# Kernel tuning notes

Measured on AMD Instinct MI355X. Metric: run time of the kernel, lower is better.

## Reference

```python
import jax, jax.numpy as jnp
import numpy as np

HIDDEN = 2048
N_HEADS = 16
N_KV_HEADS = 4
HEAD_DIM = 128
EPS = 1e-6


def rms_norm(x, w, eps=EPS):
    xf = x.astype(jnp.float32)
    var = jnp.mean(xf * xf, axis=-1, keepdims=True)
    return w * (xf * jax.lax.rsqrt(var + eps)).astype(x.dtype)


def setup_inputs() -> dict:
    key = jax.random.key(0)
    ks = jax.random.split(key, 8)
    B, S, S_ENC = 4, 2048, 1024
    inner = N_HEADS * HEAD_DIM
    kv_dim = N_KV_HEADS * HEAD_DIM
    s = 0.02
    return {
        "hidden_states": jax.random.normal(ks[0], (B, S, HIDDEN), jnp.float32),
        "encoder_hidden_states": jax.random.normal(ks[1], (B, S_ENC, HIDDEN), jnp.float32),
        "Wq": jax.random.normal(ks[2], (HIDDEN, inner), jnp.float32) * s,
        "Wk": jax.random.normal(ks[3], (HIDDEN, kv_dim), jnp.float32) * s,
        "Wv": jax.random.normal(ks[4], (HIDDEN, kv_dim), jnp.float32) * s,
        "Wo": jax.random.normal(ks[5], (inner, HIDDEN), jnp.float32) * s,
        "q_norm_w": jnp.ones((HEAD_DIM,), jnp.float32),
        "k_norm_w": jnp.ones((HEAD_DIM,), jnp.float32),
    }


def reference(hidden_states, encoder_hidden_states, Wq, Wk, Wv, Wo, q_norm_w, k_norm_w):
    B, S, _ = hidden_states.shape
    S_enc = encoder_hidden_states.shape[1]
    groups = N_HEADS // N_KV_HEADS
    scale = 1.0 / (HEAD_DIM ** 0.5)

    q = (hidden_states @ Wq).reshape(B, S, N_HEADS, HEAD_DIM)
    k = (encoder_hidden_states @ Wk).reshape(B, S_enc, N_KV_HEADS, HEAD_DIM)
    v = (encoder_hidden_states @ Wv).reshape(B, S_enc, N_KV_HEADS, HEAD_DIM)

    q = rms_norm(q, q_norm_w)
    k = rms_norm(k, k_norm_w)

    # GQA expand kv heads to full heads
    k = jnp.repeat(k, groups, axis=2)  # [B, S_enc, H, D]
    v = jnp.repeat(v, groups, axis=2)

    # non-causal SDPA
    scores = jnp.einsum("bqhd,bkhd->bhqk", q, k) * scale
    probs = jax.nn.softmax(scores, axis=-1)
    out = jnp.einsum("bhqk,bkhd->bqhd", probs, v)

    out = out.reshape(B, S, N_HEADS * HEAD_DIM)
    return out @ Wo
```

## Files before the change

### kernel.cpp

```cpp
#include <hip/hip_runtime.h>
#include <hip/hip_bf16.h>


typedef short  bf16x8 __attribute__((ext_vector_type(8)));
typedef float  f32x4  __attribute__((ext_vector_type(4)));
typedef unsigned short us;

__device__ __forceinline__ us f2bf(float f) {
    union { float f; unsigned u; } v; v.f = f;
    unsigned r = v.u + 0x7fffu + ((v.u >> 16) & 1u);
    return (us)(r >> 16);
}
__device__ __forceinline__ float bf2f(us u) {
    union { unsigned u; float f; } v; v.u = ((unsigned)u) << 16;
    return v.f;
}

typedef __attribute__((address_space(3))) unsigned int lds_u32;
typedef __attribute__((address_space(1))) const unsigned int glb_u32;

__device__ __forceinline__ void gl_lds16(const us* g, us* l) {
    __builtin_amdgcn_global_load_lds((glb_u32*)g, (lds_u32*)l, 16, 0, 0);
}

__launch_bounds__(256)
__global__ void cvt_kernel(const float* __restrict__ in, us* __restrict__ out) {
    size_t i = ((size_t)blockIdx.x * 256 + threadIdx.x) * 8;
    float4 v0 = *(const float4*)(in + i);
    float4 v1 = *(const float4*)(in + i + 4);
    bf16x8 h;
    h[0] = f2bf(v0.x); h[1] = f2bf(v0.y); h[2] = f2bf(v0.z); h[3] = f2bf(v0.w);
    h[4] = f2bf(v1.x); h[5] = f2bf(v1.y); h[6] = f2bf(v1.z); h[7] = f2bf(v1.w);
    *(bf16x8*)(out + i) = h;
}

__launch_bounds__(256)
__global__ void tpose_kernel(const float* __restrict__ in, us* __restrict__ out,
                             int K, int N) {
    __shared__ us tile[64][65];
    const int n0 = blockIdx.x * 64;
    const int k0 = blockIdx.y * 64;
    const int t  = threadIdx.x;
    const int r  = t >> 4;
    const int c4 = (t & 15) * 4;
    #pragma unroll
    for (int rr = 0; rr < 64; rr += 16) {
        float4 v = *(const float4*)(in + (size_t)(k0 + r + rr) * N + n0 + c4);
        tile[r + rr][c4 + 0] = f2bf(v.x);
        tile[r + rr][c4 + 1] = f2bf(v.y);
        tile[r + rr][c4 + 2] = f2bf(v.z);
        tile[r + rr][c4 + 3] = f2bf(v.w);
    }
    __syncthreads();
    #pragma unroll
    for (int rr = 0; rr < 64; rr += 16) {
        ushort4 o;
        o.x = tile[c4 + 0][r + rr];
        o.y = tile[c4 + 1][r + rr];
        o.z = tile[c4 + 2][r + rr];
        o.w = tile[c4 + 3][r + rr];
        *(ushort4*)(out + (size_t)(n0 + r + rr) * K + k0 + c4) = o;
    }
}

template <int EPI>
__launch_bounds__(256)
__global__ void gemm2_kernel(const us* __restrict__ A,
                             const us* __restrict__ Bt,
                             void* __restrict__ Out,
                             void* __restrict__ Out2,
                             int M, int N, int K) {
    __shared__ __align__(16) us As[128 * 64];
    __shared__ __align__(16) us Bs[128 * 64];

    const int tid  = threadIdx.x;
    const int lane = tid & 63;
    const int wv   = tid >> 6;

    const int nwg  = gridDim.x * gridDim.y;
    const int bid  = blockIdx.y * gridDim.x + blockIdx.x;
    const int cpx  = nwg >> 3;
    const int swz  = (bid & 7) * cpx + (bid >> 3);
    const int row0 = (swz / gridDim.x) * 128;
    const int n0   = (swz % gridDim.x) * 128;

    const int wr   = (wv >> 1) * 64;
    const int wc   = (wv & 1) * 64;
    const int la   = lane & 15;
    const int lg   = lane >> 4;

    const int srow = lane >> 3;
    const int scol = (((lane & 7) ^ srow) * 8);

    const int bs0 = ((0 + lg) ^ (la & 7)) * 8;
    const int bs1 = ((4 + lg) ^ (la & 7)) * 8;

    f32x4 acc[4][4] = {};

    for (int k0 = 0; k0 < K; k0 += 64) {
        #pragma unroll
        for (int r = 0; r < 4; ++r) {
            int brow = wv * 32 + r * 8;
            gl_lds16(Bt + (size_t)(n0 + brow + srow) * K + k0 + scol, &Bs[brow * 64]);
        }
        #pragma unroll
        for (int r = 0; r < 4; ++r) {
            int arow = wv * 32 + r * 8;
            gl_lds16(A + (size_t)(row0 + arow + srow) * K + k0 + scol, &As[arow * 64]);
        }
        __syncthreads();

        bf16x8 af[2][4], bg[2][4];
        #pragma unroll
        for (int i = 0; i < 4; ++i) {
            af[0][i] = *(const bf16x8*)&As[(wr + i * 16 + la) * 64 + bs0];
            af[1][i] = *(const bf16x8*)&As[(wr + i * 16 + la) * 64 + bs1];
        }
        #pragma unroll
        for (int j = 0; j < 4; ++j) {
            bg[0][j] = *(const bf16x8*)&Bs[(wc + j * 16 + la) * 64 + bs0];
            bg[1][j] = *(const bf16x8*)&Bs[(wc + j * 16 + la) * 64 + bs1];
        }
        #pragma unroll
        for (int kk = 0; kk < 2; ++kk)
            #pragma unroll
            for (int i = 0; i < 4; ++i)
                #pragma unroll
                for (int j = 0; j < 4; ++j)
                    acc[i][j] = __builtin_amdgcn_mfma_f32_16x16x32_bf16(af[kk][i], bg[kk][j], acc[i][j], 0, 0, 0);
        __syncthreads();
    }

    const int lgq = lane >> 4;
    #pragma unroll
    for (int i = 0; i < 4; ++i) {
        #pragma unroll
        for (int j = 0; j < 4; ++j) {
            #pragma unroll
            for (int r = 0; r < 4; ++r) {
                int row_g = row0 + wr + i * 16 + lgq * 4 + r;
                int col_g = n0 + wc + j * 16 + la;
                float val = acc[i][j][r];
                if (EPI == 0) {
                    ((us*)Out)[(size_t)row_g * N + col_g] = f2bf(val);
                } else if (EPI == 2) {
                    ((float*)Out)[(size_t)row_g * N + col_g] = val;
                } else {
                    if (col_g < 512) {
                        ((us*)Out)[(size_t)row_g * 512 + col_g] = f2bf(val);
                    } else {
                        int cc  = col_g - 512;
                        int b_  = row_g >> 10, s_ = row_g & 1023;
                        int kvh = cc >> 7,     d_ = cc & 127;
                        ((us*)Out2)[(((size_t)(b_ * 4 + kvh) * 128 + d_) << 10) + s_] = f2bf(val);
                    }
                }
            }
        }
    }
}

__launch_bounds__(256)
__global__ void rmsnorm_kernel(us* __restrict__ x, const float* __restrict__ w,
                               int nseg, float postscale) {
    int seg  = blockIdx.x * 4 + (threadIdx.x >> 6);
    if (seg >= nseg) return;
    int lane = threadIdx.x & 63;
    size_t base = (size_t)seg * 128 + lane * 2;
    unsigned v = *(const unsigned*)&x[base];
    float x0 = bf2f((us)(v & 0xffff));
    float x1 = bf2f((us)(v >> 16));
    float s = x0 * x0 + x1 * x1;
    #pragma unroll
    for (int m = 1; m < 64; m <<= 1) s += __shfl_xor(s, m, 64);
    float rinv = rsqrtf(s * (1.0f / 128.0f) + 1e-6f) * postscale;
    x0 = x0 * rinv * w[lane * 2];
    x1 = x1 * rinv * w[lane * 2 + 1];
    unsigned o = (unsigned)f2bf(x0) | ((unsigned)f2bf(x1) << 16);
    *(unsigned*)&x[base] = o;
}

__launch_bounds__(256, 2)
__global__ void attn_kernel(const us* __restrict__ Q,
                            const us* __restrict__ Kb,
                            const us* __restrict__ Vt,
                            us* __restrict__ Ob) {
    __shared__ __align__(16) us Klds[64 * 132];
    __shared__ __align__(16) us Vtlds[128 * 68];
    __shared__ __align__(16) us Plds[4][32 * 68];

    const int tid  = threadIdx.x;
    const int bid  = blockIdx.x;
    const int qt   = bid & 15;
    const int bh   = bid >> 4;
    const int b    = bh >> 4;
    const int h    = bh & 15;
    const int kvh  = h >> 2;

    const int lane = tid & 63;
    const int wv   = tid >> 6;
    const int la   = lane & 15;
    const int lg   = lane >> 4;
    const int lb   = lg * 8;

    const int qr0 = qt * 128 + wv * 32;

    bf16x8 aq[2][4];
    #pragma unroll
    for (int i = 0; i < 2; ++i)
        #pragma unroll
        for (int t = 0; t < 4; ++t)
            aq[i][t] = *(const bf16x8*)&Q[(size_t)(b * 2048 + qr0 + i * 16 + la) * 2048
                                          + h * 128 + t * 32 + lb];

    f32x4 oacc[2][8] = {};
    float l_part[2][4] = {};

    const us* Kbase  = Kb + (size_t)(b * 1024) * 512 + kvh * 128;
    const us* Vtbase = Vt + (size_t)(b * 4 + kvh) * 128 * 1024;

    for (int kt = 0; kt < 16; ++kt) {
        #pragma unroll
        for (int r = 0; r < 4; ++r) {
            int idx  = tid + r * 256;
            int srow = idx >> 4;
            int c8   = (idx & 15) << 3;
            uint4 v = *(const uint4*)(Kbase + (size_t)(kt * 64 + srow) * 512 + c8);
            *(uint4*)&Klds[srow * 132 + c8] = v;
        }
        #pragma unroll
        for (int r = 0; r < 4; ++r) {
            int idx  = tid + r * 256;
            int drow = idx >> 3;
            int c8   = (idx & 7) << 3;
            uint4 v = *(const uint4*)(Vtbase + (size_t)drow * 1024 + kt * 64 + c8);
            *(uint4*)&Vtlds[drow * 68 + c8] = v;
        }
        __syncthreads();

        f32x4 sacc[2][4] = {};
        __builtin_amdgcn_s_setprio(1);
        #pragma unroll
        for (int j = 0; j < 4; ++j) {
            bf16x8 bk[4];
            #pragma unroll
            for (int t = 0; t < 4; ++t)
                bk[t] = *(const bf16x8*)&Klds[(j * 16 + la) * 132 + t * 32 + lb];
            #pragma unroll
            for (int t = 0; t < 4; ++t)
                #pragma unroll
                for (int i = 0; i < 2; ++i)
                    sacc[i][j] = __builtin_amdgcn_mfma_f32_16x16x32_bf16(aq[i][t], bk[t], sacc[i][j], 0, 0, 0);
        }
        __builtin_amdgcn_s_setprio(0);

        #pragma unroll
        for (int i = 0; i < 2; ++i) {
            #pragma unroll
            for (int r = 0; r < 4; ++r) {
                float ls = 0.0f;
                #pragma unroll
                for (int j = 0; j < 4; ++j) {
                    float p = __expf(sacc[i][j][r]);
                    sacc[i][j][r] = p;
                    ls += p;
                }
                l_part[i][r] += ls;
            }
        }

        #pragma unroll
        for (int i = 0; i < 2; ++i)
            #pragma unroll
            for (int j = 0; j < 4; ++j)
                #pragma unroll
                for (int r = 0; r < 4; ++r)
                    Plds[wv][(i * 16 + lg * 4 + r) * 68 + j * 16 + la] = f2bf(sacc[i][j][r]);

        __builtin_amdgcn_s_setprio(1);
        #pragma unroll
        for (int ks = 0; ks < 2; ++ks) {
            bf16x8 pa[2];
            #pragma unroll
            for (int i = 0; i < 2; ++i)
                pa[i] = *(const bf16x8*)&Plds[wv][(i * 16 + la) * 68 + ks * 32 + lb];
            #pragma unroll
            for (int df = 0; df < 8; ++df) {
                bf16x8 bv = *(const bf16x8*)&Vtlds[(df * 16 + la) * 68 + ks * 32 + lb];
                #pragma unroll
                for (int i = 0; i < 2; ++i)
                    oacc[i][df] = __builtin_amdgcn_mfma_f32_16x16x32_bf16(pa[i], bv, oacc[i][df], 0, 0, 0);
            }
        }
        __builtin_amdgcn_s_setprio(0);
        __syncthreads();
    }

    #pragma unroll
    for (int i = 0; i < 2; ++i) {
        #pragma unroll
        for (int r = 0; r < 4; ++r) {
            float l = l_part[i][r];
            l += __shfl_xor(l, 1, 64);
            l += __shfl_xor(l, 2, 64);
            l += __shfl_xor(l, 4, 64);
            l += __shfl_xor(l, 8, 64);
            float inv = 1.0f / l;
            int row_g = b * 2048 + qr0 + i * 16 + lg * 4 + r;
            #pragma unroll
            for (int df = 0; df < 8; ++df) {
                int col_g = h * 128 + df * 16 + la;
                Ob[(size_t)row_g * 2048 + col_g] = f2bf(oacc[i][df][r] * inv);
            }
        }
    }
}

extern "C" void kernel_launch(void* const* d_in, const int* in_sizes, int n_in,
                              void* d_out, int out_size, void* d_ws, size_t ws_size,
                              hipStream_t stream) {
    const float* hidden = (const float*)d_in[0];
    const float* enc    = (const float*)d_in[1];
    const float* Wq     = (const float*)d_in[2];
    const float* Wk     = (const float*)d_in[3];
    const float* Wv     = (const float*)d_in[4];
    const float* Wo     = (const float*)d_in[5];
    const float* qw     = (const float*)d_in[6];
    const float* kw     = (const float*)d_in[7];
    float* out = (float*)d_out;

    us* ws16 = (us*)d_ws;
    us* hidden_bf = ws16;
    us* WqT       = ws16 + 16777216;
    us* Qu        = ws16 + 20971520;
    us* enc_bf    = ws16;
    us* WkT       = ws16 + 8388608;
    us* WvT       = ws16 + 9437184;
    us* WoT       = ws16 + 10485760;
    us* Kn        = ws16 + 14680064;
    us* Vt        = ws16 + 16777216;

    dim3 blk(256);
    const float scale = 0.08838834764831845f;

    cvt_kernel<<<dim3(8192), blk, 0, stream>>>(hidden, hidden_bf);
    tpose_kernel<<<dim3(32, 32), blk, 0, stream>>>(Wq, WqT, 2048, 2048);
    gemm2_kernel<0><<<dim3(16, 64), blk, 0, stream>>>(hidden_bf, WqT, Qu, nullptr, 8192, 2048, 2048);

    cvt_kernel<<<dim3(4096), blk, 0, stream>>>(enc, enc_bf);
    tpose_kernel<<<dim3(8, 32),  blk, 0, stream>>>(Wk, WkT, 2048, 512);
    tpose_kernel<<<dim3(8, 32),  blk, 0, stream>>>(Wv, WvT, 2048, 512);
    tpose_kernel<<<dim3(32, 32), blk, 0, stream>>>(Wo, WoT, 2048, 2048);
    gemm2_kernel<3><<<dim3(8, 32), blk, 0, stream>>>(enc_bf, WkT, Kn, Vt, 4096, 1024, 2048);

    rmsnorm_kernel<<<dim3(32768), blk, 0, stream>>>(Qu, qw, 8192 * 16, scale);
    rmsnorm_kernel<<<dim3(4096),  blk, 0, stream>>>(Kn, kw, 4096 * 4, 1.0f);

    attn_kernel<<<dim3(1024), blk, 0, stream>>>(Qu, Kn, Vt, Qu);

    gemm2_kernel<2><<<dim3(16, 64), blk, 0, stream>>>(Qu, WoT, out, nullptr, 8192, 2048, 2048);
}
```

Measured before the change: 374.4 us.

## Read V directly from global memory, fold log2e into Q scale, pack bf16 converts

Stops staging the transposed V tile in shared memory; each lane now loads its V fragments for the PV MFMAs straight from global memory, which cuts LDS footprint and store traffic at the cost of uncached, latency-exposed global loads inside the MFMA loop. The softmax exponent switches from __expf to the native exp2 builtin, with log2(e) folded into the Q rmsnorm post-scale so the math is unchanged. Probability conversion to bf16 uses the packed v_cvt_pk_bf16_f32 instruction for two values at once instead of manual rounding.

Result: slower. 472.7 us (+26.3%).

```diff
diff --git a/kernel.cpp b/kernel.cpp
--- a/kernel.cpp
+++ b/kernel.cpp
@@ -186,7 +186,6 @@
                             const us* __restrict__ Vt,
                             us* __restrict__ Ob) {
     __shared__ __align__(16) us Klds[64 * 132];
-    __shared__ __align__(16) us Vtlds[128 * 68];
     __shared__ __align__(16) us Plds[4][32 * 68];
 
     const int tid  = threadIdx.x;
@@ -218,6 +217,7 @@
 
     const us* Kbase  = Kb + (size_t)(b * 1024) * 512 + kvh * 128;
     const us* Vtbase = Vt + (size_t)(b * 4 + kvh) * 128 * 1024;
+    const us* Vlane  = Vtbase + (size_t)la * 1024 + lb;
 
     for (int kt = 0; kt < 16; ++kt) {
         #pragma unroll
@@ -228,14 +228,6 @@
             uint4 v = *(const uint4*)(Kbase + (size_t)(kt * 64 + srow) * 512 + c8);
             *(uint4*)&Klds[srow * 132 + c8] = v;
         }
-        #pragma unroll
-        for (int r = 0; r < 4; ++r) {
-            int idx  = tid + r * 256;
-            int drow = idx >> 3;
-            int c8   = (idx & 7) << 3;
-            uint4 v = *(const uint4*)(Vtbase + (size_t)drow * 1024 + kt * 64 + c8);
-            *(uint4*)&Vtlds[drow * 68 + c8] = v;
-        }
         __syncthreads();
 
         f32x4 sacc[2][4] = {};
@@ -261,7 +253,7 @@
                 float ls = 0.0f;
                 #pragma unroll
                 for (int j = 0; j < 4; ++j) {
-                    float p = __expf(sacc[i][j][r]);
+                    float p = __builtin_amdgcn_exp2f(sacc[i][j][r]);
                     sacc[i][j][r] = p;
                     ls += p;
                 }
@@ -270,12 +262,20 @@
         }
 
         #pragma unroll
-        for (int i = 0; i < 2; ++i)
-            #pragma unroll
-            for (int j = 0; j < 4; ++j)
-                #pragma unroll
-                for (int r = 0; r < 4; ++r)
-                    Plds[wv][(i * 16 + lg * 4 + r) * 68 + j * 16 + la] = f2bf(sacc[i][j][r]);
+        for (int i = 0; i < 2; ++i) {
+            #pragma unroll
+            for (int r = 0; r < 4; ++r) {
+                int prow = (i * 16 + lg * 4 + r) * 68;
+                #pragma unroll
+                for (int j = 0; j < 4; j += 2) {
+                    unsigned pk;
+                    asm("v_cvt_pk_bf16_f32 %0, %1, %2"
+                        : "=v"(pk) : "v"(sacc[i][j][r]), "v"(sacc[i][j + 1][r]));
+                    Plds[wv][prow + j * 16 + la]       = (us)(pk & 0xffffu);
+                    Plds[wv][prow + (j + 1) * 16 + la] = (us)(pk >> 16);
+                }
+            }
+        }
 
         __builtin_amdgcn_s_setprio(1);
         #pragma unroll
@@ -286,7 +286,8 @@
                 pa[i] = *(const bf16x8*)&Plds[wv][(i * 16 + la) * 68 + ks * 32 + lb];
             #pragma unroll
             for (int df = 0; df < 8; ++df) {
-                bf16x8 bv = *(const bf16x8*)&Vtlds[(df * 16 + la) * 68 + ks * 32 + lb];
+                bf16x8 bv = *(const bf16x8*)(Vlane + (size_t)df * 16384
+                                             + kt * 64 + ks * 32);
                 #pragma unroll
                 for (int i = 0; i < 2; ++i)
                     oacc[i][df] = __builtin_amdgcn_mfma_f32_16x16x32_bf16(pa[i], bv, oacc[i][df], 0, 0, 0);
@@ -341,7 +342,7 @@
     us* Vt        = ws16 + 16777216;
 
     dim3 blk(256);
-    const float scale = 0.08838834764831845f;
+    const float qscale = 0.08838834764831845f * 1.4426950408889634f;
 
     cvt_kernel<<<dim3(8192), blk, 0, stream>>>(hidden, hidden_bf);
     tpose_kernel<<<dim3(32, 32), blk, 0, stream>>>(Wq, WqT, 2048, 2048);
@@ -353,7 +354,7 @@
     tpose_kernel<<<dim3(32, 32), blk, 0, stream>>>(Wo, WoT, 2048, 2048);
     gemm2_kernel<3><<<dim3(8, 32), blk, 0, stream>>>(enc_bf, WkT, Kn, Vt, 4096, 1024, 2048);
 
-    rmsnorm_kernel<<<dim3(32768), blk, 0, stream>>>(Qu, qw, 8192 * 16, scale);
+    rmsnorm_kernel<<<dim3(32768), blk, 0, stream>>>(Qu, qw, 8192 * 16, qscale);
     rmsnorm_kernel<<<dim3(4096),  blk, 0, stream>>>(Kn, kw, 4096 * 4, 1.0f);
 
     attn_kernel<<<dim3(1024), blk, 0, stream>>>(Qu, Kn, Vt, Qu);
```
